# Kernel optimization log

Measured on AMD Instinct MI355X. Metric: run time of the kernel, lower is better.

The kernel has to match this reference:

```python
import jax, jax.numpy as jnp
import numpy as np

N_NODES = 50000
IN_CH, HID_CH, OUT_CH = 128, 128, 64
N_EDGES = 800000


def setup_inputs() -> dict:
    key = jax.random.key(0)
    k = jax.random.split(key, 6)
    x = jax.random.normal(k[0], (N_NODES, IN_CH), dtype=jnp.float32)
    edge_index = jax.random.randint(k[1], (2, N_EDGES), 0, N_NODES, dtype=jnp.int64)
    # Glorot-ish init for weights
    W1 = jax.random.normal(k[2], (IN_CH, HID_CH), dtype=jnp.float32) * (1.0 / np.sqrt(IN_CH))
    b1 = jnp.zeros((HID_CH,), dtype=jnp.float32)
    W2 = jax.random.normal(k[3], (HID_CH, OUT_CH), dtype=jnp.float32) * (1.0 / np.sqrt(HID_CH))
    b2 = jnp.zeros((OUT_CH,), dtype=jnp.float32)
    return {"x": x, "edge_index": edge_index, "W1": W1, "b1": b1, "W2": W2, "b2": b2}


def _gcn_conv(x, src, dst, W, b, n_nodes):
    """PyG GCNConv: linear, add self-loops, symmetric deg^-1/2 normalization, scatter-add."""
    h = x @ W  # [N, F_out]
    loop = jnp.arange(n_nodes, dtype=src.dtype)
    s = jnp.concatenate([src, loop])  # [E+N]
    d = jnp.concatenate([dst, loop])
    # in-degree on target nodes (including self-loops), edge weight = 1
    deg = jnp.zeros((n_nodes,), dtype=h.dtype).at[d].add(1.0)
    dinv = jnp.where(deg > 0, jax.lax.rsqrt(deg), 0.0)
    norm = dinv[s] * dinv[d]  # [E+N]
    msg = h[s] * norm[:, None]  # [E+N, F_out]
    out = jax.ops.segment_sum(msg, d, num_segments=n_nodes)
    return out + b


def reference(x, edge_index, W1, b1, W2, b2):
    src, dst = edge_index[0], edge_index[1]
    h = _gcn_conv(x, src, dst, W1, b1, N_NODES)
    h = jax.nn.relu(h)
    # dropout in eval mode -> identity
    out = _gcn_conv(h, src, dst, W2, b2, N_NODES)
    return out
```

## Files before the change

### kernel.cpp

```cpp
#include <hip/hip_runtime.h>

typedef __attribute__((ext_vector_type(8))) short bf16x8;
typedef __attribute__((ext_vector_type(4))) float f32x4;

constexpr int NN = 50000;
constexpr int NE = 800000;
constexpr int C1 = 128;
constexpr int C2 = 64;
constexpr int NBK = 196;
constexpr int EPB = 2048;
constexpr int NBLK = (NE + EPB - 1) / EPB;
constexpr int MT = NN / 16;
constexpr int MMB = 500;
constexpr int MMWAVES = MMB * 4;
constexpr int CAP = 8192;
constexpr int GNB = (NN + 63) / 64;

__device__ __forceinline__ unsigned short f2bf(float f) {
    unsigned int u = __float_as_uint(f);
    u += 0x7FFFu + ((u >> 16) & 1u);
    return (unsigned short)(u >> 16);
}
__device__ __forceinline__ float2 bf2f(unsigned int u) {
    return make_float2(__uint_as_float(u << 16), __uint_as_float(u & 0xFFFF0000u));
}
__device__ __forceinline__ bf16x8 pack8(float4 a, float4 b) {
    bf16x8 r;
    r[0] = (short)f2bf(a.x); r[1] = (short)f2bf(a.y);
    r[2] = (short)f2bf(a.z); r[3] = (short)f2bf(a.w);
    r[4] = (short)f2bf(b.x); r[5] = (short)f2bf(b.y);
    r[6] = (short)f2bf(b.z); r[7] = (short)f2bf(b.w);
    return r;
}
__device__ __forceinline__ void addrow(float* a, uint4 v) {
    float2 p;
    p = bf2f(v.x); a[0] += p.x; a[1] += p.y;
    p = bf2f(v.y); a[2] += p.x; a[3] += p.y;
    p = bf2f(v.z); a[4] += p.x; a[5] += p.y;
    p = bf2f(v.w); a[6] += p.x; a[7] += p.y;
}

__global__ __launch_bounds__(256) void bin_kernel(const int* __restrict__ src,
                                                  const int* __restrict__ dst,
                                                  unsigned int* __restrict__ ebuf,
                                                  int* __restrict__ localOff) {
    __shared__ int lhist[NBK];
    __shared__ int ls[256];
    __shared__ int lcur[NBK];
    __shared__ unsigned int lbuf[EPB];
    const int t = threadIdx.x;
    const int base = blockIdx.x * EPB;
    if (t < NBK) lhist[t] = 0;
    __syncthreads();
    int b[8]; unsigned int p[8];
    #pragma unroll
    for (int i = 0; i < 8; i++) {
        int e = base + i * 256 + t;
        if (e < NE) {
            int s = src[e], d = dst[e];
            b[i] = d >> 8;
            p[i] = ((unsigned int)(d & 255) << 16) | (unsigned int)s;
            atomicAdd(&lhist[b[i]], 1);
        } else b[i] = -1;
    }
    __syncthreads();
    int v = (t < NBK) ? lhist[t] : 0;
    ls[t] = v;
    __syncthreads();
    #pragma unroll
    for (int d = 1; d < 256; d <<= 1) {
        int u = (t >= d) ? ls[t - d] : 0;
        __syncthreads();
        ls[t] += u;
        __syncthreads();
    }
    if (t < NBK) {
        lcur[t] = ls[t] - v;
        localOff[blockIdx.x * 200 + t] = ls[t] - v;
    }
    if (t == NBK - 1) localOff[blockIdx.x * 200 + NBK] = ls[t];
    __syncthreads();
    #pragma unroll
    for (int i = 0; i < 8; i++) {
        if (b[i] >= 0) {
            int lp = atomicAdd(&lcur[b[i]], 1);
            lbuf[lp] = p[i];
        }
    }
    __syncthreads();
    #pragma unroll
    for (int i = 0; i < 8; i++)
        ebuf[base + i * 256 + t] = lbuf[i * 256 + t];
}

__global__ __launch_bounds__(256) void place_kernel(const unsigned int* __restrict__ ebuf,
                                                    const int* __restrict__ localOff,
                                                    unsigned short* __restrict__ esrc,
                                                    int* __restrict__ cnt,
                                                    int* __restrict__ off,
                                                    float* __restrict__ dinv) {
    __shared__ unsigned int lbuf[CAP];
    __shared__ int lhist[256];
    __shared__ int ls[256];
    __shared__ int lcur[256];
    __shared__ int red[256];
    const int t = threadIdx.x;
    const int bkt = blockIdx.x;
    const int node0 = bkt << 8;
    const int nnodes = min(256, NN - node0);

    const int j0 = 2 * t, j1 = 2 * t + 1;
    int s0 = 0, l0 = 0, s1 = 0, l1 = 0;
    if (j0 < NBLK) { s0 = localOff[j0 * 200 + bkt]; l0 = localOff[j0 * 200 + bkt + 1] - s0; }
    if (j1 < NBLK) { s1 = localOff[j1 * 200 + bkt]; l1 = localOff[j1 * 200 + bkt + 1] - s1; }

    red[t] = s0 + s1;
    ls[t] = l0 + l1;
    lhist[t] = 0;
    __syncthreads();
    #pragma unroll
    for (int d = 1; d < 256; d <<= 1) {
        int u = (t >= d) ? ls[t - d] : 0;
        int r = (t + d < 256) ? red[t + d] : 0;
        __syncthreads();
        ls[t] += u;
        red[t] += r;
        __syncthreads();
    }
    const int segBase = red[0];
    const int total = ls[255];
    const int base0 = ls[t] - (l0 + l1);
    const int base1 = base0 + l0;
    const bool fits = (total <= CAP);

    if (fits) {
        const unsigned int* q0 = ebuf + j0 * EPB + s0;
        for (int k = 0; k < l0; k++) lbuf[base0 + k] = q0[k];
        const unsigned int* q1 = ebuf + j1 * EPB + s1;
        for (int k = 0; k < l1; k++) lbuf[base1 + k] = q1[k];
        __syncthreads();
        for (int k = t; k < total; k += 256) atomicAdd(&lhist[lbuf[k] >> 16], 1);
    } else {
        const unsigned int* q0 = ebuf + j0 * EPB + s0;
        for (int k = 0; k < l0; k++) atomicAdd(&lhist[q0[k] >> 16], 1);
        const unsigned int* q1 = ebuf + j1 * EPB + s1;
        for (int k = 0; k < l1; k++) atomicAdd(&lhist[q1[k] >> 16], 1);
    }
    __syncthreads();
    int v = lhist[t];
    ls[t] = v;
    __syncthreads();
    #pragma unroll
    for (int d = 1; d < 256; d <<= 1) {
        int u = (t >= d) ? ls[t - d] : 0;
        __syncthreads();
        ls[t] += u;
        __syncthreads();
    }
    int ex = ls[t] - v;
    lcur[t] = ex;
    if (t < nnodes) {
        cnt[node0 + t] = v;
        off[node0 + t] = segBase + ex;
        dinv[node0 + t] = rsqrtf((float)v + 1.0f);
    }
    __syncthreads();
    if (fits) {
        for (int k = t; k < total; k += 256) {
            unsigned int pp = lbuf[k];
            int lp = atomicAdd(&lcur[pp >> 16], 1);
            esrc[segBase + lp] = (unsigned short)(pp & 0xFFFFu);
        }
    } else {
        const unsigned int* q0 = ebuf + j0 * EPB + s0;
        for (int k = 0; k < l0; k++) {
            unsigned int pp = q0[k];
            int lp = atomicAdd(&lcur[pp >> 16], 1);
            esrc[segBase + lp] = (unsigned short)(pp & 0xFFFFu);
        }
        const unsigned int* q1 = ebuf + j1 * EPB + s1;
        for (int k = 0; k < l1; k++) {
            unsigned int pp = q1[k];
            int lp = atomicAdd(&lcur[pp >> 16], 1);
            esrc[segBase + lp] = (unsigned short)(pp & 0xFFFFu);
        }
    }
}

__global__ __launch_bounds__(256, 2) void mm1_kernel(const float* __restrict__ x,
                                                     const float* __restrict__ W,
                                                     const float* __restrict__ dinv,
                                                     unsigned short* __restrict__ g1) {
    __shared__ unsigned short wl[4][8][64][8];
    const int t = threadIdx.x;
    for (int i = 0; i < 64; i++) {
        int idx = i * 256 + t;
        int k = idx >> 7, n = idx & 127;
        wl[k >> 5][n >> 4][((k >> 3) & 3) * 16 + (n & 15)][k & 7] = f2bf(W[idx]);
    }
    __syncthreads();
    const int lane = t & 63, lm = lane & 15, quad = lane >> 4;

    bf16x8 bfr[4][8];
    #pragma unroll
    for (int s = 0; s < 4; s++)
        #pragma unroll
        for (int nt = 0; nt < 8; nt++)
            bfr[s][nt] = *(const bf16x8*)&wl[s][nt][lane][0];

    int wg = blockIdx.x * 4 + (t >> 6);
    for (int tile = wg; tile < MT; tile += MMWAVES) {
        int row0 = tile << 4;
        const float* xr = x + (size_t)(row0 + lm) * 128 + quad * 8;
        bf16x8 af[4];
        #pragma unroll
        for (int s = 0; s < 4; s++) {
            float4 p = *(const float4*)(xr + s * 32);
            float4 q = *(const float4*)(xr + s * 32 + 4);
            af[s] = pack8(p, q);
        }
        f32x4 acc[8];
        #pragma unroll
        for (int nt = 0; nt < 8; nt++) acc[nt] = (f32x4){0.f, 0.f, 0.f, 0.f};
        #pragma unroll
        for (int s = 0; s < 4; s++)
            #pragma unroll
            for (int nt = 0; nt < 8; nt++)
                acc[nt] = __builtin_amdgcn_mfma_f32_16x16x32_bf16(af[s], bfr[s][nt],
                                                                  acc[nt], 0, 0, 0);
        float4 dv = *(const float4*)(dinv + row0 + quad * 4);
        float dvv[4] = {dv.x, dv.y, dv.z, dv.w};
        #pragma unroll
        for (int nt = 0; nt < 8; nt++)
            #pragma unroll
            for (int r = 0; r < 4; r++)
                g1[(size_t)(row0 + quad * 4 + r) * 128 + nt * 16 + lm] =
                    f2bf(acc[nt][r] * dvv[r]);
    }
}

__global__ __launch_bounds__(256, 2) void mm2_kernel(const unsigned short* __restrict__ x2,
                                                     const float* __restrict__ W,
                                                     const float* __restrict__ dinv,
                                                     unsigned short* __restrict__ g2) {
    __shared__ unsigned short wl[4][4][64][8];
    const int t = threadIdx.x;
    for (int i = 0; i < 32; i++) {
        int idx = i * 256 + t;
        int k = idx >> 6, n = idx & 63;
        wl[k >> 5][n >> 4][((k >> 3) & 3) * 16 + (n & 15)][k & 7] = f2bf(W[idx]);
    }
    __syncthreads();
    const int lane = t & 63, lm = lane & 15, quad = lane >> 4;

    bf16x8 bfr[4][4];
    #pragma unroll
    for (int s = 0; s < 4; s++)
        #pragma unroll
        for (int nt = 0; nt < 4; nt++)
            bfr[s][nt] = *(const bf16x8*)&wl[s][nt][lane][0];

    int wg = blockIdx.x * 4 + (t >> 6);
    for (int tile = wg; tile < MT; tile += MMWAVES) {
        int row0 = tile << 4;
        const bf16x8* xr = (const bf16x8*)(x2 + (size_t)(row0 + lm) * 128 + quad * 8);
        bf16x8 af[4];
        #pragma unroll
        for (int s = 0; s < 4; s++) af[s] = xr[s * 4];
        f32x4 acc[4];
        #pragma unroll
        for (int nt = 0; nt < 4; nt++) acc[nt] = (f32x4){0.f, 0.f, 0.f, 0.f};
        #pragma unroll
        for (int s = 0; s < 4; s++)
            #pragma unroll
            for (int nt = 0; nt < 4; nt++)
                acc[nt] = __builtin_amdgcn_mfma_f32_16x16x32_bf16(af[s], bfr[s][nt],
                                                                  acc[nt], 0, 0, 0);
        float4 dv = *(const float4*)(dinv + row0 + quad * 4);
        float dvv[4] = {dv.x, dv.y, dv.z, dv.w};
        #pragma unroll
        for (int nt = 0; nt < 4; nt++)
            #pragma unroll
            for (int r = 0; r < 4; r++)
                g2[(size_t)(row0 + quad * 4 + r) * 64 + nt * 16 + lm] =
                    f2bf(acc[nt][r] * dvv[r]);
    }
}

__global__ __launch_bounds__(256) void gather1_kernel(const unsigned short* __restrict__ g1,
                                                      const unsigned short* __restrict__ esrc,
                                                      const int* __restrict__ off,
                                                      const int* __restrict__ cnt,
                                                      const float* __restrict__ dinv,
                                                      const float* __restrict__ b1,
                                                      unsigned short* __restrict__ x2) {
    const int slice = blockIdx.x & 3;
    const int n = (blockIdx.x >> 2) * 64 + (threadIdx.x >> 2);
    if (n >= NN) return;
    const int p = threadIdx.x & 3;
    const int col = slice * 4 + p;
    const uint4* G = (const uint4*)g1;
    float a0[8] = {0,0,0,0,0,0,0,0};
    float a1[8] = {0,0,0,0,0,0,0,0};
    addrow(a0, G[(size_t)n * 16 + col]);
    int s0 = off[n], c = cnt[n];
    int i = 0;
    for (; i + 1 < c; i += 2) {
        int sA = esrc[s0 + i];
        int sB = esrc[s0 + i + 1];
        uint4 vA = G[(size_t)sA * 16 + col];
        uint4 vB = G[(size_t)sB * 16 + col];
        addrow(a0, vA);
        addrow(a1, vB);
    }
    if (i < c) addrow(a0, G[(size_t)esrc[s0 + i] * 16 + col]);
    #pragma unroll
    for (int j = 0; j < 8; j++) a0[j] += a1[j];
    float sc = dinv[n];
    float4 bA = ((const float4*)b1)[col * 2];
    float4 bB = ((const float4*)b1)[col * 2 + 1];
    float4 pp = make_float4(fmaxf(sc * a0[0] + bA.x, 0.f), fmaxf(sc * a0[1] + bA.y, 0.f),
                            fmaxf(sc * a0[2] + bA.z, 0.f), fmaxf(sc * a0[3] + bA.w, 0.f));
    float4 qq = make_float4(fmaxf(sc * a0[4] + bB.x, 0.f), fmaxf(sc * a0[5] + bB.y, 0.f),
                            fmaxf(sc * a0[6] + bB.z, 0.f), fmaxf(sc * a0[7] + bB.w, 0.f));
    *(bf16x8*)(x2 + (size_t)n * 128 + col * 8) = pack8(pp, qq);
}

__global__ __launch_bounds__(256) void gather2_kernel(const unsigned short* __restrict__ g2,
                                                      const unsigned short* __restrict__ esrc,
                                                      const int* __restrict__ off,
                                                      const int* __restrict__ cnt,
                                                      const float* __restrict__ dinv,
                                                      const float* __restrict__ b2,
                                                      float* __restrict__ out) {
    const int slice = blockIdx.x & 1;
    const int n = (blockIdx.x >> 1) * 64 + (threadIdx.x >> 2);
    if (n >= NN) return;
    const int p = threadIdx.x & 3;
    const int col = slice * 4 + p;
    const uint4* G = (const uint4*)g2;
    float a0[8] = {0,0,0,0,0,0,0,0};
    float a1[8] = {0,0,0,0,0,0,0,0};
    addrow(a0, G[(size_t)n * 8 + col]);
    int s0 = off[n], c = cnt[n];
    int i = 0;
    for (; i + 1 < c; i += 2) {
        int sA = esrc[s0 + i];
        int sB = esrc[s0 + i + 1];
        uint4 vA = G[(size_t)sA * 8 + col];
        uint4 vB = G[(size_t)sB * 8 + col];
        addrow(a0, vA);
        addrow(a1, vB);
    }
    if (i < c) addrow(a0, G[(size_t)esrc[s0 + i] * 8 + col]);
    #pragma unroll
    for (int j = 0; j < 8; j++) a0[j] += a1[j];
    float sc = dinv[n];
    float4 bA = ((const float4*)b2)[col * 2];
    float4 bB = ((const float4*)b2)[col * 2 + 1];
    float* o = out + (size_t)n * 64 + col * 8;
    *(float4*)o = make_float4(sc * a0[0] + bA.x, sc * a0[1] + bA.y,
                              sc * a0[2] + bA.z, sc * a0[3] + bA.w);
    *(float4*)(o + 4) = make_float4(sc * a0[4] + bB.x, sc * a0[5] + bB.y,
                                    sc * a0[6] + bB.z, sc * a0[7] + bB.w);
}

extern "C" void kernel_launch(void* const* d_in, const int* in_sizes, int n_in,
                              void* d_out, int out_size, void* d_ws, size_t ws_size,
                              hipStream_t stream) {
    const float* x  = (const float*)d_in[0];
    const int* edges = (const int*)d_in[1];
    const float* W1 = (const float*)d_in[2];
    const float* b1 = (const float*)d_in[3];
    const float* W2 = (const float*)d_in[4];
    const float* b2 = (const float*)d_in[5];
    const int* src = edges;
    const int* dst = edges + NE;

    int* localOff  = (int*)d_ws;
    unsigned int* ebuf = (unsigned int*)(localOff + 78208);
    unsigned short* esrc = (unsigned short*)(ebuf + (size_t)NBLK * EPB);
    int* cnt       = (int*)(esrc + 800768);
    int* off       = cnt + 50048;
    float* dinv    = (float*)(off + 50048);
    unsigned short* g1 = (unsigned short*)(dinv + 50048);
    unsigned short* x2 = g1 + (size_t)NN * C1;
    unsigned short* g2 = g1;
    float* out = (float*)d_out;

    bin_kernel<<<NBLK, 256, 0, stream>>>(src, dst, ebuf, localOff);
    place_kernel<<<NBK, 256, 0, stream>>>(ebuf, localOff, esrc, cnt, off, dinv);

    mm1_kernel<<<MMB, 256, 0, stream>>>(x, W1, dinv, g1);
    gather1_kernel<<<GNB * 4, 256, 0, stream>>>(g1, esrc, off, cnt, dinv, b1, x2);

    mm2_kernel<<<MMB, 256, 0, stream>>>(x2, W2, dinv, g2);
    gather2_kernel<<<GNB * 2, 256, 0, stream>>>(g2, esrc, off, cnt, dinv, b2, out);
}
```

Measured before the change: 183.8 us.

## Overlap first matmul with edge binning by fusing into heterogeneous kernels

New measurement: 200.9 us. 1.09x slower.

```diff
diff --git a/kernel.cpp b/kernel.cpp
--- a/kernel.cpp
+++ b/kernel.cpp
@@ -11,10 +11,14 @@
 constexpr int EPB = 2048;
 constexpr int NBLK = (NE + EPB - 1) / EPB;
 constexpr int MT = NN / 16;
-constexpr int MMB = 500;
-constexpr int MMWAVES = MMB * 4;
 constexpr int CAP = 8192;
 constexpr int GNB = (NN + 63) / 64;
+
+constexpr int MM_A = 250;
+constexpr int MM_B = 250;
+constexpr int TSPLIT = 1562;
+constexpr int MMB2 = 500;
+constexpr int MM2WAVES = MMB2 * 4;
 
 __device__ __forceinline__ unsigned short f2bf(float f) {
     unsigned int u = __float_as_uint(f);
@@ -39,18 +43,34 @@
     p = bf2f(v.z); a[4] += p.x; a[5] += p.y;
     p = bf2f(v.w); a[6] += p.x; a[7] += p.y;
 }
-
-__global__ __launch_bounds__(256) void bin_kernel(const int* __restrict__ src,
-                                                  const int* __restrict__ dst,
-                                                  unsigned int* __restrict__ ebuf,
-                                                  int* __restrict__ localOff) {
-    __shared__ int lhist[NBK];
-    __shared__ int ls[256];
-    __shared__ int lcur[NBK];
-    __shared__ unsigned int lbuf[EPB];
+__device__ __forceinline__ void fmarow(float* a, uint4 v, float s) {
+    float2 p;
+    p = bf2f(v.x); a[0] = fmaf(p.x, s, a[0]); a[1] = fmaf(p.y, s, a[1]);
+    p = bf2f(v.y); a[2] = fmaf(p.x, s, a[2]); a[3] = fmaf(p.y, s, a[3]);
+    p = bf2f(v.z); a[4] = fmaf(p.x, s, a[4]); a[5] = fmaf(p.y, s, a[5]);
+    p = bf2f(v.w); a[6] = fmaf(p.x, s, a[6]); a[7] = fmaf(p.y, s, a[7]);
+}
+
+struct BinSmem {
+    int lhist[NBK];
+    int ls[256];
+    int lcur[NBK];
+    unsigned int lbuf[EPB];
+};
+struct PlaceSmem {
+    unsigned int lbuf[CAP];
+    int lhist[256];
+    int ls[256];
+    int lcur[256];
+    int red[256];
+};
+
+__device__ void bin_work(const int* __restrict__ src, const int* __restrict__ dst,
+                         unsigned int* __restrict__ ebuf, int* __restrict__ localOff,
+                         BinSmem& S) {
     const int t = threadIdx.x;
     const int base = blockIdx.x * EPB;
-    if (t < NBK) lhist[t] = 0;
+    if (t < NBK) S.lhist[t] = 0;
     __syncthreads();
     int b[8]; unsigned int p[8];
     #pragma unroll
@@ -60,50 +80,46 @@
             int s = src[e], d = dst[e];
             b[i] = d >> 8;
             p[i] = ((unsigned int)(d & 255) << 16) | (unsigned int)s;
-            atomicAdd(&lhist[b[i]], 1);
+            atomicAdd(&S.lhist[b[i]], 1);
         } else b[i] = -1;
     }
     __syncthreads();
-    int v = (t < NBK) ? lhist[t] : 0;
-    ls[t] = v;
+    int v = (t < NBK) ? S.lhist[t] : 0;
+    S.ls[t] = v;
     __syncthreads();
     #pragma unroll
     for (int d = 1; d < 256; d <<= 1) {
-        int u = (t >= d) ? ls[t - d] : 0;
-        __syncthreads();
-        ls[t] += u;
+        int u = (t >= d) ? S.ls[t - d] : 0;
+        __syncthreads();
+        S.ls[t] += u;
         __syncthreads();
     }
     if (t < NBK) {
-        lcur[t] = ls[t] - v;
-        localOff[blockIdx.x * 200 + t] = ls[t] - v;
-    }
-    if (t == NBK - 1) localOff[blockIdx.x * 200 + NBK] = ls[t];
+        S.lcur[t] = S.ls[t] - v;
+        localOff[blockIdx.x * 200 + t] = S.ls[t] - v;
+    }
+    if (t == NBK - 1) localOff[blockIdx.x * 200 + NBK] = S.ls[t];
     __syncthreads();
     #pragma unroll
     for (int i = 0; i < 8; i++) {
         if (b[i] >= 0) {
-            int lp = atomicAdd(&lcur[b[i]], 1);
-            lbuf[lp] = p[i];
+            int lp = atomicAdd(&S.lcur[b[i]], 1);
+            S.lbuf[lp] = p[i];
         }
     }
     __syncthreads();
     #pragma unroll
     for (int i = 0; i < 8; i++)
-        ebuf[base + i * 256 + t] = lbuf[i * 256 + t];
-}
-
-__global__ __launch_bounds__(256) void place_kernel(const unsigned int* __restrict__ ebuf,
-                                                    const int* __restrict__ localOff,
-                                                    unsigned short* __restrict__ esrc,
-                                                    int* __restrict__ cnt,
-                                                    int* __restrict__ off,
-                                                    float* __restrict__ dinv) {
-    __shared__ unsigned int lbuf[CAP];
-    __shared__ int lhist[256];
-    __shared__ int ls[256];
-    __shared__ int lcur[256];
-    __shared__ int red[256];
+        ebuf[base + i * 256 + t] = S.lbuf[i * 256 + t];
+}
+
+__device__ void place_work(const unsigned int* __restrict__ ebuf,
+                           const int* __restrict__ localOff,
+                           unsigned short* __restrict__ esrc,
+                           int* __restrict__ cnt,
+                           int* __restrict__ off,
+                           float* __restrict__ dinv,
+                           PlaceSmem& S) {
     const int t = threadIdx.x;
     const int bkt = blockIdx.x;
     const int node0 = bkt << 8;
@@ -114,51 +130,51 @@
     if (j0 < NBLK) { s0 = localOff[j0 * 200 + bkt]; l0 = localOff[j0 * 200 + bkt + 1] - s0; }
     if (j1 < NBLK) { s1 = localOff[j1 * 200 + bkt]; l1 = localOff[j1 * 200 + bkt + 1] - s1; }
 
-    red[t] = s0 + s1;
-    ls[t] = l0 + l1;
-    lhist[t] = 0;
+    S.red[t] = s0 + s1;
+    S.ls[t] = l0 + l1;
+    S.lhist[t] = 0;
     __syncthreads();
     #pragma unroll
     for (int d = 1; d < 256; d <<= 1) {
-        int u = (t >= d) ? ls[t - d] : 0;
-        int r = (t + d < 256) ? red[t + d] : 0;
-        __syncthreads();
-        ls[t] += u;
-        red[t] += r;
-        __syncthreads();
-    }
-    const int segBase = red[0];
-    const int total = ls[255];
-    const int base0 = ls[t] - (l0 + l1);
+        int u = (t >= d) ? S.ls[t - d] : 0;
+        int r = (t + d < 256) ? S.red[t + d] : 0;
+        __syncthreads();
+        S.ls[t] += u;
+        S.red[t] += r;
+        __syncthreads();
+    }
+    const int segBase = S.red[0];
+    const int total = S.ls[255];
+    const int base0 = S.ls[t] - (l0 + l1);
     const int base1 = base0 + l0;
     const bool fits = (total <= CAP);
 
     if (fits) {
         const unsigned int* q0 = ebuf + j0 * EPB + s0;
-        for (int k = 0; k < l0; k++) lbuf[base0 + k] = q0[k];
+        for (int k = 0; k < l0; k++) S.lbuf[base0 + k] = q0[k];
         const unsigned int* q1 = ebuf + j1 * EPB + s1;
-        for (int k = 0; k < l1; k++) lbuf[base1 + k] = q1[k];
-        __syncthreads();
-        for (int k = t; k < total; k += 256) atomicAdd(&lhist[lbuf[k] >> 16], 1);
+        for (int k = 0; k < l1; k++) S.lbuf[base1 + k] = q1[k];
+        __syncthreads();
+        for (int k = t; k < total; k += 256) atomicAdd(&S.lhist[S.lbuf[k] >> 16], 1);
     } else {
         const unsigned int* q0 = ebuf + j0 * EPB + s0;
-        for (int k = 0; k < l0; k++) atomicAdd(&lhist[q0[k] >> 16], 1);
+        for (int k = 0; k < l0; k++) atomicAdd(&S.lhist[q0[k] >> 16], 1);
         const unsigned int* q1 = ebuf + j1 * EPB + s1;
-        for (int k = 0; k < l1; k++) atomicAdd(&lhist[q1[k] >> 16], 1);
-    }
-    __syncthreads();
-    int v = lhist[t];
-    ls[t] = v;
+        for (int k = 0; k < l1; k++) atomicAdd(&S.lhist[q1[k] >> 16], 1);
+    }
+    __syncthreads();
+    int v = S.lhist[t];
+    S.ls[t] = v;
     __syncthreads();
     #pragma unroll
     for (int d = 1; d < 256; d <<= 1) {
-        int u = (t >= d) ? ls[t - d] : 0;
-        __syncthreads();
-        ls[t] += u;
-        __syncthreads();
-    }
-    int ex = ls[t] - v;
-    lcur[t] = ex;
+        int u = (t >= d) ? S.ls[t - d] : 0;
+        __syncthreads();
+        S.ls[t] += u;
+        __syncthreads();
+    }
+    int ex = S.ls[t] - v;
+    S.lcur[t] = ex;
     if (t < nnodes) {
         cnt[node0 + t] = v;
         off[node0 + t] = segBase + ex;
@@ -167,31 +183,30 @@
     __syncthreads();
     if (fits) {
         for (int k = t; k < total; k += 256) {
-            unsigned int pp = lbuf[k];
-            int lp = atomicAdd(&lcur[pp >> 16], 1);
+            unsigned int pp = S.lbuf[k];
+            int lp = atomicAdd(&S.lcur[pp >> 16], 1);
             esrc[segBase + lp] = (unsigned short)(pp & 0xFFFFu);
         }
     } else {
         const unsigned int* q0 = ebuf + j0 * EPB + s0;
         for (int k = 0; k < l0; k++) {
             unsigned int pp = q0[k];
-            int lp = atomicAdd(&lcur[pp >> 16], 1);
+            int lp = atomicAdd(&S.lcur[pp >> 16], 1);
             esrc[segBase + lp] = (unsigned short)(pp & 0xFFFFu);
         }
         const unsigned int* q1 = ebuf + j1 * EPB + s1;
         for (int k = 0; k < l1; k++) {
             unsigned int pp = q1[k];
-            int lp = atomicAdd(&lcur[pp >> 16], 1);
+            int lp = atomicAdd(&S.lcur[pp >> 16], 1);
             esrc[segBase + lp] = (unsigned short)(pp & 0xFFFFu);
         }
     }
 }
 
-__global__ __launch_bounds__(256, 2) void mm1_kernel(const float* __restrict__ x,
-                                                     const float* __restrict__ W,
-                                                     const float* __restrict__ dinv,
-                                                     unsigned short* __restrict__ g1) {
-    __shared__ unsigned short wl[4][8][64][8];
+__device__ void mm1_work(const float* __restrict__ x, const float* __restrict__ W,
+                         unsigned short* __restrict__ g1,
+                         unsigned short (&wl)[4][8][64][8],
+                         int mblk, int nwaves, int tile0, int tile1) {
     const int t = threadIdx.x;
     for (int i = 0; i < 64; i++) {
         int idx = i * 256 + t;
@@ -208,8 +223,8 @@
         for (int nt = 0; nt < 8; nt++)
             bfr[s][nt] = *(const bf16x8*)&wl[s][nt][lane][0];
 
-    int wg = blockIdx.x * 4 + (t >> 6);
-    for (int tile = wg; tile < MT; tile += MMWAVES) {
+    int wg = mblk * 4 + (t >> 6);
+    for (int tile = tile0 + wg; tile < tile1; tile += nwaves) {
         int row0 = tile << 4;
         const float* xr = x + (size_t)(row0 + lm) * 128 + quad * 8;
         bf16x8 af[4];
@@ -228,15 +243,44 @@
             for (int nt = 0; nt < 8; nt++)
                 acc[nt] = __builtin_amdgcn_mfma_f32_16x16x32_bf16(af[s], bfr[s][nt],
                                                                   acc[nt], 0, 0, 0);
-        float4 dv = *(const float4*)(dinv + row0 + quad * 4);
-        float dvv[4] = {dv.x, dv.y, dv.z, dv.w};
         #pragma unroll
         for (int nt = 0; nt < 8; nt++)
             #pragma unroll
             for (int r = 0; r < 4; r++)
-                g1[(size_t)(row0 + quad * 4 + r) * 128 + nt * 16 + lm] =
-                    f2bf(acc[nt][r] * dvv[r]);
-    }
+                g1[(size_t)(row0 + quad * 4 + r) * 128 + nt * 16 + lm] = f2bf(acc[nt][r]);
+    }
+}
+
+__global__ __launch_bounds__(256, 2) void fusedA_kernel(const int* __restrict__ src,
+                                                        const int* __restrict__ dst,
+                                                        unsigned int* __restrict__ ebuf,
+                                                        int* __restrict__ localOff,
+                                                        const float* __restrict__ x,
+                                                        const float* __restrict__ W1,
+                                                        unsigned short* __restrict__ g1) {
+    __shared__ union { BinSmem b; unsigned short wl[4][8][64][8]; } sm;
+    if (blockIdx.x < NBLK) {
+        bin_work(src, dst, ebuf, localOff, sm.b);
+        return;
+    }
+    mm1_work(x, W1, g1, sm.wl, blockIdx.x - NBLK, MM_A * 4, 0, TSPLIT);
+}
+
+__global__ __launch_bounds__(256, 2) void fusedB_kernel(const unsigned int* __restrict__ ebuf,
+                                                        const int* __restrict__ localOff,
+                                                        unsigned short* __restrict__ esrc,
+                                                        int* __restrict__ cnt,
+                                                        int* __restrict__ off,
+                                                        float* __restrict__ dinv,
+                                                        const float* __restrict__ x,
+                                                        const float* __restrict__ W1,
+                                                        unsigned short* __restrict__ g1) {
+    __shared__ union { PlaceSmem p; unsigned short wl[4][8][64][8]; } sm;
+    if (blockIdx.x < NBK) {
+        place_work(ebuf, localOff, esrc, cnt, off, dinv, sm.p);
+        return;
+    }
+    mm1_work(x, W1, g1, sm.wl, blockIdx.x - NBK, MM_B * 4, TSPLIT, MT);
 }
 
 __global__ __launch_bounds__(256, 2) void mm2_kernel(const unsigned short* __restrict__ x2,
@@ -261,7 +305,7 @@
             bfr[s][nt] = *(const bf16x8*)&wl[s][nt][lane][0];
 
     int wg = blockIdx.x * 4 + (t >> 6);
-    for (int tile = wg; tile < MT; tile += MMWAVES) {
+    for (int tile = wg; tile < MT; tile += MM2WAVES) {
         int row0 = tile << 4;
         const bf16x8* xr = (const bf16x8*)(x2 + (size_t)(row0 + lm) * 128 + quad * 8);
         bf16x8 af[4];
@@ -302,21 +346,26 @@
     const uint4* G = (const uint4*)g1;
     float a0[8] = {0,0,0,0,0,0,0,0};
     float a1[8] = {0,0,0,0,0,0,0,0};
-    addrow(a0, G[(size_t)n * 16 + col]);
+    float sc = dinv[n];
+    fmarow(a0, G[(size_t)n * 16 + col], sc);
     int s0 = off[n], c = cnt[n];
     int i = 0;
     for (; i + 1 < c; i += 2) {
         int sA = esrc[s0 + i];
         int sB = esrc[s0 + i + 1];
+        float dA = dinv[sA];
+        float dB = dinv[sB];
         uint4 vA = G[(size_t)sA * 16 + col];
         uint4 vB = G[(size_t)sB * 16 + col];
-        addrow(a0, vA);
-        addrow(a1, vB);
-    }
-    if (i < c) addrow(a0, G[(size_t)esrc[s0 + i] * 16 + col]);
+        fmarow(a0, vA, dA);
+        fmarow(a1, vB, dB);
+    }
+    if (i < c) {
+        int sA = esrc[s0 + i];
+        fmarow(a0, G[(size_t)sA * 16 + col], dinv[sA]);
+    }
     #pragma unroll
     for (int j = 0; j < 8; j++) a0[j] += a1[j];
-    float sc = dinv[n];
     float4 bA = ((const float4*)b1)[col * 2];
     float4 bB = ((const float4*)b1)[col * 2 + 1];
     float4 pp = make_float4(fmaxf(sc * a0[0] + bA.x, 0.f), fmaxf(sc * a0[1] + bA.y, 0.f),
@@ -388,12 +437,11 @@
     unsigned short* g2 = g1;
     float* out = (float*)d_out;
 
-    bin_kernel<<<NBLK, 256, 0, stream>>>(src, dst, ebuf, localOff);
-    place_kernel<<<NBK, 256, 0, stream>>>(ebuf, localOff, esrc, cnt, off, dinv);
-
-    mm1_kernel<<<MMB, 256, 0, stream>>>(x, W1, dinv, g1);
+    fusedA_kernel<<<NBLK + MM_A, 256, 0, stream>>>(src, dst, ebuf, localOff, x, W1, g1);
+    fusedB_kernel<<<NBK + MM_B, 256, 0, stream>>>(ebuf, localOff, esrc, cnt, off, dinv,
+                                                  x, W1, g1);
     gather1_kernel<<<GNB * 4, 256, 0, stream>>>(g1, esrc, off, cnt, dinv, b1, x2);
 
-    mm2_kernel<<<MMB, 256, 0, stream>>>(x2, W2, dinv, g2);
+    mm2_kernel<<<MMB2, 256, 0, stream>>>(x2, W2, dinv, g2);
     gather2_kernel<<<GNB * 2, 256, 0, stream>>>(g2, esrc, off, cnt, dinv, b2, out);
 }
```

## Slice-major g1/g2 layout with XCC-affine dynamic work assignment in gathers

Applied to the files above, without the earlier changes.

Measured after the change: 257.5 us. +40.1%, slower.

```diff
diff --git a/kernel.cpp b/kernel.cpp
--- a/kernel.cpp
+++ b/kernel.cpp
@@ -14,7 +14,8 @@
 constexpr int MMB = 500;
 constexpr int MMWAVES = MMB * 4;
 constexpr int CAP = 8192;
-constexpr int GNB = (NN + 63) / 64;
+constexpr int CH1 = (NN + 127) / 128;
+constexpr int CH2 = (NN + 255) / 256;
 
 __device__ __forceinline__ unsigned short f2bf(float f) {
     unsigned int u = __float_as_uint(f);
@@ -40,16 +41,35 @@
     p = bf2f(v.w); a[6] += p.x; a[7] += p.y;
 }
 
+template <int CHUNKS>
+__device__ __forceinline__ void pick_work(int* qc, int* sh2) {
+    if (threadIdx.x == 0) {
+        unsigned xcc;
+        asm volatile("s_getreg_b32 %0, hwreg(HW_REG_XCC_ID)" : "=s"(xcc));
+        int sl = (int)(xcc & 7u), ch = -1;
+        #pragma unroll
+        for (int a = 0; a < 8; a++) {
+            int s2 = (sl + a) & 7;
+            int c = atomicAdd(&qc[s2], 1);
+            if (c < CHUNKS) { sl = s2; ch = c; break; }
+        }
+        sh2[0] = sl; sh2[1] = ch;
+    }
+    __syncthreads();
+}
+
 __global__ __launch_bounds__(256) void bin_kernel(const int* __restrict__ src,
                                                   const int* __restrict__ dst,
                                                   unsigned int* __restrict__ ebuf,
-                                                  int* __restrict__ localOff) {
+                                                  int* __restrict__ localOff,
+                                                  int* __restrict__ qc) {
     __shared__ int lhist[NBK];
     __shared__ int ls[256];
     __shared__ int lcur[NBK];
     __shared__ unsigned int lbuf[EPB];
     const int t = threadIdx.x;
     const int base = blockIdx.x * EPB;
+    if (blockIdx.x == 0 && t < 16) qc[t] = 0;
     if (t < NBK) lhist[t] = 0;
     __syncthreads();
     int b[8]; unsigned int p[8];
@@ -234,7 +254,7 @@
         for (int nt = 0; nt < 8; nt++)
             #pragma unroll
             for (int r = 0; r < 4; r++)
-                g1[(size_t)(row0 + quad * 4 + r) * 128 + nt * 16 + lm] =
+                g1[(size_t)nt * (NN * 16) + (size_t)(row0 + quad * 4 + r) * 16 + lm] =
                     f2bf(acc[nt][r] * dvv[r]);
     }
 }
@@ -282,7 +302,8 @@
         for (int nt = 0; nt < 4; nt++)
             #pragma unroll
             for (int r = 0; r < 4; r++)
-                g2[(size_t)(row0 + quad * 4 + r) * 64 + nt * 16 + lm] =
+                g2[(size_t)(nt * 2 + (lm >> 3)) * (NN * 8) +
+                   (size_t)(row0 + quad * 4 + r) * 8 + (lm & 7)] =
                     f2bf(acc[nt][r] * dvv[r]);
     }
 }
@@ -293,37 +314,42 @@
                                                       const int* __restrict__ cnt,
                                                       const float* __restrict__ dinv,
                                                       const float* __restrict__ b1,
-                                                      unsigned short* __restrict__ x2) {
-    const int slice = blockIdx.x & 3;
-    const int n = (blockIdx.x >> 2) * 64 + (threadIdx.x >> 2);
+                                                      unsigned short* __restrict__ x2,
+                                                      int* __restrict__ qc) {
+    __shared__ int sh2[2];
+    pick_work<CH1>(qc, sh2);
+    const int slice = sh2[0], chunk = sh2[1];
+    if (chunk < 0) return;
+    const int n = chunk * 128 + (threadIdx.x >> 1);
     if (n >= NN) return;
-    const int p = threadIdx.x & 3;
-    const int col = slice * 4 + p;
-    const uint4* G = (const uint4*)g1;
+    const int p = threadIdx.x & 1;
+    const uint4* G = (const uint4*)(g1 + (size_t)slice * (NN * 16));
     float a0[8] = {0,0,0,0,0,0,0,0};
     float a1[8] = {0,0,0,0,0,0,0,0};
-    addrow(a0, G[(size_t)n * 16 + col]);
+    addrow(a0, G[(size_t)n * 2 + p]);
     int s0 = off[n], c = cnt[n];
     int i = 0;
     for (; i + 1 < c; i += 2) {
         int sA = esrc[s0 + i];
         int sB = esrc[s0 + i + 1];
-        uint4 vA = G[(size_t)sA * 16 + col];
-        uint4 vB = G[(size_t)sB * 16 + col];
+        uint4 vA = G[(size_t)sA * 2 + p];
+        uint4 vB = G[(size_t)sB * 2 + p];
         addrow(a0, vA);
         addrow(a1, vB);
     }
-    if (i < c) addrow(a0, G[(size_t)esrc[s0 + i] * 16 + col]);
+    if (i < c) addrow(a0, G[(size_t)esrc[s0 + i] * 2 + p]);
     #pragma unroll
     for (int j = 0; j < 8; j++) a0[j] += a1[j];
     float sc = dinv[n];
-    float4 bA = ((const float4*)b1)[col * 2];
-    float4 bB = ((const float4*)b1)[col * 2 + 1];
+    const int ch0 = slice * 16 + p * 8;
+    float4 bA = *(const float4*)(b1 + ch0);
+    float4 bB = *(const float4*)(b1 + ch0 + 4);
     float4 pp = make_float4(fmaxf(sc * a0[0] + bA.x, 0.f), fmaxf(sc * a0[1] + bA.y, 0.f),
                             fmaxf(sc * a0[2] + bA.z, 0.f), fmaxf(sc * a0[3] + bA.w, 0.f));
     float4 qq = make_float4(fmaxf(sc * a0[4] + bB.x, 0.f), fmaxf(sc * a0[5] + bB.y, 0.f),
                             fmaxf(sc * a0[6] + bB.z, 0.f), fmaxf(sc * a0[7] + bB.w, 0.f));
-    *(bf16x8*)(x2 + (size_t)n * 128 + col * 8) = pack8(pp, qq);
+    bf16x8 vout = pack8(pp, qq);
+    __builtin_nontemporal_store(vout, (bf16x8*)(x2 + (size_t)n * 128 + ch0));
 }
 
 __global__ __launch_bounds__(256) void gather2_kernel(const unsigned short* __restrict__ g2,
@@ -332,37 +358,42 @@
                                                       const int* __restrict__ cnt,
                                                       const float* __restrict__ dinv,
                                                       const float* __restrict__ b2,
-                                                      float* __restrict__ out) {
-    const int slice = blockIdx.x & 1;
-    const int n = (blockIdx.x >> 1) * 64 + (threadIdx.x >> 2);
+                                                      float* __restrict__ out,
+                                                      int* __restrict__ qc) {
+    __shared__ int sh2[2];
+    pick_work<CH2>(qc, sh2);
+    const int slice = sh2[0], chunk = sh2[1];
+    if (chunk < 0) return;
+    const int n = chunk * 256 + threadIdx.x;
     if (n >= NN) return;
-    const int p = threadIdx.x & 3;
-    const int col = slice * 4 + p;
-    const uint4* G = (const uint4*)g2;
+    const uint4* G = (const uint4*)(g2 + (size_t)slice * (NN * 8));
     float a0[8] = {0,0,0,0,0,0,0,0};
     float a1[8] = {0,0,0,0,0,0,0,0};
-    addrow(a0, G[(size_t)n * 8 + col]);
+    addrow(a0, G[n]);
     int s0 = off[n], c = cnt[n];
     int i = 0;
     for (; i + 1 < c; i += 2) {
         int sA = esrc[s0 + i];
         int sB = esrc[s0 + i + 1];
-        uint4 vA = G[(size_t)sA * 8 + col];
-        uint4 vB = G[(size_t)sB * 8 + col];
+        uint4 vA = G[sA];
+        uint4 vB = G[sB];
         addrow(a0, vA);
         addrow(a1, vB);
     }
-    if (i < c) addrow(a0, G[(size_t)esrc[s0 + i] * 8 + col]);
+    if (i < c) addrow(a0, G[esrc[s0 + i]]);
     #pragma unroll
     for (int j = 0; j < 8; j++) a0[j] += a1[j];
     float sc = dinv[n];
-    float4 bA = ((const float4*)b2)[col * 2];
-    float4 bB = ((const float4*)b2)[col * 2 + 1];
-    float* o = out + (size_t)n * 64 + col * 8;
-    *(float4*)o = make_float4(sc * a0[0] + bA.x, sc * a0[1] + bA.y,
-                              sc * a0[2] + bA.z, sc * a0[3] + bA.w);
-    *(float4*)(o + 4) = make_float4(sc * a0[4] + bB.x, sc * a0[5] + bB.y,
-                                    sc * a0[6] + bB.z, sc * a0[7] + bB.w);
+    const int ch0 = slice * 8;
+    float4 bA = *(const float4*)(b2 + ch0);
+    float4 bB = *(const float4*)(b2 + ch0 + 4);
+    float* o = out + (size_t)n * 64 + ch0;
+    f32x4 o0 = {sc * a0[0] + bA.x, sc * a0[1] + bA.y,
+                sc * a0[2] + bA.z, sc * a0[3] + bA.w};
+    f32x4 o1 = {sc * a0[4] + bB.x, sc * a0[5] + bB.y,
+                sc * a0[6] + bB.z, sc * a0[7] + bB.w};
+    __builtin_nontemporal_store(o0, (f32x4*)o);
+    __builtin_nontemporal_store(o1, (f32x4*)(o + 4));
 }
 
 extern "C" void kernel_launch(void* const* d_in, const int* in_sizes, int n_in,
@@ -383,17 +414,18 @@
     int* cnt       = (int*)(esrc + 800768);
     int* off       = cnt + 50048;
     float* dinv    = (float*)(off + 50048);
-    unsigned short* g1 = (unsigned short*)(dinv + 50048);
+    int* qc        = (int*)(dinv + 50048);
+    unsigned short* g1 = (unsigned short*)(qc + 16);
     unsigned short* x2 = g1 + (size_t)NN * C1;
     unsigned short* g2 = g1;
     float* out = (float*)d_out;
 
-    bin_kernel<<<NBLK, 256, 0, stream>>>(src, dst, ebuf, localOff);
+    bin_kernel<<<NBLK, 256, 0, stream>>>(src, dst, ebuf, localOff, qc);
     place_kernel<<<NBK, 256, 0, stream>>>(ebuf, localOff, esrc, cnt, off, dinv);
 
     mm1_kernel<<<MMB, 256, 0, stream>>>(x, W1, dinv, g1);
-    gather1_kernel<<<GNB * 4, 256, 0, stream>>>(g1, esrc, off, cnt, dinv, b1, x2);
+    gather1_kernel<<<8 * CH1, 256, 0, stream>>>(g1, esrc, off, cnt, dinv, b1, x2, qc);
 
     mm2_kernel<<<MMB, 256, 0, stream>>>(x2, W2, dinv, g2);
-    gather2_kernel<<<GNB * 2, 256, 0, stream>>>(g2, esrc, off, cnt, dinv, b2, out);
-}
+    gather2_kernel<<<8 * CH2, 256, 0, stream>>>(g2, esrc, off, cnt, dinv, b2, out, qc + 8);
+}
```

## Assign one wavefront per node in gather kernels with shuffled neighbor indices

Applied to the files above, without the earlier changes.

After: 182.8 us. Within noise of the previous version (-0.5%).

```diff
diff --git a/kernel.cpp b/kernel.cpp
--- a/kernel.cpp
+++ b/kernel.cpp
@@ -14,7 +14,7 @@
 constexpr int MMB = 500;
 constexpr int MMWAVES = MMB * 4;
 constexpr int CAP = 8192;
-constexpr int GNB = (NN + 63) / 64;
+constexpr int GB = (NN + 3) / 4;
 
 __device__ __forceinline__ unsigned short f2bf(float f) {
     unsigned int u = __float_as_uint(f);
@@ -31,13 +31,6 @@
     r[4] = (short)f2bf(b.x); r[5] = (short)f2bf(b.y);
     r[6] = (short)f2bf(b.z); r[7] = (short)f2bf(b.w);
     return r;
-}
-__device__ __forceinline__ void addrow(float* a, uint4 v) {
-    float2 p;
-    p = bf2f(v.x); a[0] += p.x; a[1] += p.y;
-    p = bf2f(v.y); a[2] += p.x; a[3] += p.y;
-    p = bf2f(v.z); a[4] += p.x; a[5] += p.y;
-    p = bf2f(v.w); a[6] += p.x; a[7] += p.y;
 }
 
 __global__ __launch_bounds__(256) void bin_kernel(const int* __restrict__ src,
@@ -294,36 +287,46 @@
                                                       const float* __restrict__ dinv,
                                                       const float* __restrict__ b1,
                                                       unsigned short* __restrict__ x2) {
-    const int slice = blockIdx.x & 3;
-    const int n = (blockIdx.x >> 2) * 64 + (threadIdx.x >> 2);
+    const int n = blockIdx.x * 4 + (threadIdx.x >> 6);
     if (n >= NN) return;
-    const int p = threadIdx.x & 3;
-    const int col = slice * 4 + p;
-    const uint4* G = (const uint4*)g1;
-    float a0[8] = {0,0,0,0,0,0,0,0};
-    float a1[8] = {0,0,0,0,0,0,0,0};
-    addrow(a0, G[(size_t)n * 16 + col]);
-    int s0 = off[n], c = cnt[n];
-    int i = 0;
-    for (; i + 1 < c; i += 2) {
-        int sA = esrc[s0 + i];
-        int sB = esrc[s0 + i + 1];
-        uint4 vA = G[(size_t)sA * 16 + col];
-        uint4 vB = G[(size_t)sB * 16 + col];
-        addrow(a0, vA);
-        addrow(a1, vB);
-    }
-    if (i < c) addrow(a0, G[(size_t)esrc[s0 + i] * 16 + col]);
-    #pragma unroll
-    for (int j = 0; j < 8; j++) a0[j] += a1[j];
-    float sc = dinv[n];
-    float4 bA = ((const float4*)b1)[col * 2];
-    float4 bB = ((const float4*)b1)[col * 2 + 1];
-    float4 pp = make_float4(fmaxf(sc * a0[0] + bA.x, 0.f), fmaxf(sc * a0[1] + bA.y, 0.f),
-                            fmaxf(sc * a0[2] + bA.z, 0.f), fmaxf(sc * a0[3] + bA.w, 0.f));
-    float4 qq = make_float4(fmaxf(sc * a0[4] + bB.x, 0.f), fmaxf(sc * a0[5] + bB.y, 0.f),
-                            fmaxf(sc * a0[6] + bB.z, 0.f), fmaxf(sc * a0[7] + bB.w, 0.f));
-    *(bf16x8*)(x2 + (size_t)n * 128 + col * 8) = pack8(pp, qq);
+    const int lane = threadIdx.x & 63;
+    const unsigned int* G = (const unsigned int*)g1;
+    float2 ps = bf2f(G[(size_t)n * 64 + lane]);
+    float a0 = ps.x, a1 = ps.y;
+    float c0 = 0.f, c1 = 0.f;
+    const int s0 = off[n], c = cnt[n];
+    for (int base = 0; base < c; base += 64) {
+        const int m = min(64, c - base);
+        int vidx = 0;
+        if (lane < m) vidx = esrc[s0 + base + lane];
+        int i = 0;
+        for (; i + 3 < m; i += 4) {
+            int sA = __shfl(vidx, i);
+            int sB = __shfl(vidx, i + 1);
+            int sC = __shfl(vidx, i + 2);
+            int sD = __shfl(vidx, i + 3);
+            unsigned int vA = G[(size_t)sA * 64 + lane];
+            unsigned int vB = G[(size_t)sB * 64 + lane];
+            unsigned int vC = G[(size_t)sC * 64 + lane];
+            unsigned int vD = G[(size_t)sD * 64 + lane];
+            float2 pA = bf2f(vA); a0 += pA.x; a1 += pA.y;
+            float2 pB = bf2f(vB); c0 += pB.x; c1 += pB.y;
+            float2 pC = bf2f(vC); a0 += pC.x; a1 += pC.y;
+            float2 pD = bf2f(vD); c0 += pD.x; c1 += pD.y;
+        }
+        for (; i < m; i++) {
+            int sA = __shfl(vidx, i);
+            float2 pA = bf2f(G[(size_t)sA * 64 + lane]);
+            a0 += pA.x; a1 += pA.y;
+        }
+    }
+    a0 += c0; a1 += c1;
+    const float sc = dinv[n];
+    const float2 bb = ((const float2*)b1)[lane];
+    const float o0 = fmaxf(sc * a0 + bb.x, 0.f);
+    const float o1 = fmaxf(sc * a1 + bb.y, 0.f);
+    const unsigned int uo = (unsigned int)f2bf(o0) | ((unsigned int)f2bf(o1) << 16);
+    ((unsigned int*)x2)[(size_t)n * 64 + lane] = uo;
 }
 
 __global__ __launch_bounds__(256) void gather2_kernel(const unsigned short* __restrict__ g2,
@@ -333,36 +336,40 @@
                                                       const float* __restrict__ dinv,
                                                       const float* __restrict__ b2,
                                                       float* __restrict__ out) {
-    const int slice = blockIdx.x & 1;
-    const int n = (blockIdx.x >> 1) * 64 + (threadIdx.x >> 2);
+    const int n = blockIdx.x * 4 + (threadIdx.x >> 6);
     if (n >= NN) return;
-    const int p = threadIdx.x & 3;
-    const int col = slice * 4 + p;
-    const uint4* G = (const uint4*)g2;
-    float a0[8] = {0,0,0,0,0,0,0,0};
-    float a1[8] = {0,0,0,0,0,0,0,0};
-    addrow(a0, G[(size_t)n * 8 + col]);
-    int s0 = off[n], c = cnt[n];
-    int i = 0;
-    for (; i + 1 < c; i += 2) {
-        int sA = esrc[s0 + i];
-        int sB = esrc[s0 + i + 1];
-        uint4 vA = G[(size_t)sA * 8 + col];
-        uint4 vB = G[(size_t)sB * 8 + col];
-        addrow(a0, vA);
-        addrow(a1, vB);
-    }
-    if (i < c) addrow(a0, G[(size_t)esrc[s0 + i] * 8 + col]);
-    #pragma unroll
-    for (int j = 0; j < 8; j++) a0[j] += a1[j];
-    float sc = dinv[n];
-    float4 bA = ((const float4*)b2)[col * 2];
-    float4 bB = ((const float4*)b2)[col * 2 + 1];
-    float* o = out + (size_t)n * 64 + col * 8;
-    *(float4*)o = make_float4(sc * a0[0] + bA.x, sc * a0[1] + bA.y,
-                              sc * a0[2] + bA.z, sc * a0[3] + bA.w);
-    *(float4*)(o + 4) = make_float4(sc * a0[4] + bB.x, sc * a0[5] + bB.y,
-                                    sc * a0[6] + bB.z, sc * a0[7] + bB.w);
+    const int lane = threadIdx.x & 63;
+    const unsigned short* G = g2;
+    float a0 = __uint_as_float((unsigned int)G[(size_t)n * 64 + lane] << 16);
+    float c0 = 0.f;
+    const int s0 = off[n], c = cnt[n];
+    for (int base = 0; base < c; base += 64) {
+        const int m = min(64, c - base);
+        int vidx = 0;
+        if (lane < m) vidx = esrc[s0 + base + lane];
+        int i = 0;
+        for (; i + 3 < m; i += 4) {
+            int sA = __shfl(vidx, i);
+            int sB = __shfl(vidx, i + 1);
+            int sC = __shfl(vidx, i + 2);
+            int sD = __shfl(vidx, i + 3);
+            unsigned short vA = G[(size_t)sA * 64 + lane];
+            unsigned short vB = G[(size_t)sB * 64 + lane];
+            unsigned short vC = G[(size_t)sC * 64 + lane];
+            unsigned short vD = G[(size_t)sD * 64 + lane];
+            a0 += __uint_as_float((unsigned int)vA << 16);
+            c0 += __uint_as_float((unsigned int)vB << 16);
+            a0 += __uint_as_float((unsigned int)vC << 16);
+            c0 += __uint_as_float((unsigned int)vD << 16);
+        }
+        for (; i < m; i++) {
+            int sA = __shfl(vidx, i);
+            a0 += __uint_as_float((unsigned int)G[(size_t)sA * 64 + lane] << 16);
+        }
+    }
+    a0 += c0;
+    const float sc = dinv[n];
+    out[(size_t)n * 64 + lane] = sc * a0 + b2[lane];
 }
 
 extern "C" void kernel_launch(void* const* d_in, const int* in_sizes, int n_in,
@@ -392,8 +399,8 @@
     place_kernel<<<NBK, 256, 0, stream>>>(ebuf, localOff, esrc, cnt, off, dinv);
 
     mm1_kernel<<<MMB, 256, 0, stream>>>(x, W1, dinv, g1);
-    gather1_kernel<<<GNB * 4, 256, 0, stream>>>(g1, esrc, off, cnt, dinv, b1, x2);
+    gather1_kernel<<<GB, 256, 0, stream>>>(g1, esrc, off, cnt, dinv, b1, x2);
 
     mm2_kernel<<<MMB, 256, 0, stream>>>(x2, W2, dinv, g2);
-    gather2_kernel<<<GNB * 2, 256, 0, stream>>>(g2, esrc, off, cnt, dinv, b2, out);
-}
+    gather2_kernel<<<GB, 256, 0, stream>>>(g2, esrc, off, cnt, dinv, b2, out);
+}
```
